# Optimization experiments

Hardware: AMD Instinct MI355X
Metric: run time of the kernel (lower is better)

## Reference

```python
import jax, jax.numpy as jnp
import numpy as np

K = 3          # number of nearest neighbors for interpolation
EPS = 1e-8     # inverse-distance epsilon
BN_EPS = 1e-5  # torch BatchNorm1d default eps

B, NY, NX = 4, 16384, 4096
CY, CX = 128, 256
DIM = CY + CX
SHARED = (512, 256, 128)


def setup_inputs() -> dict:
    key = jax.random.key(0)
    ks = jax.random.split(key, 16)
    inp = {
        'y_points': jax.random.normal(ks[0], (B, NY, 3), jnp.float32),
        'y_feats': jax.random.normal(ks[1], (B, NY, CY), jnp.float32),
        'x_points': jax.random.normal(ks[2], (B, NX, 3), jnp.float32),
        'x_feats': jax.random.normal(ks[3], (B, NX, CX), jnp.float32),
    }
    in_chs = (DIM,) + SHARED[:-1]
    for i, (cin, cout) in enumerate(zip(in_chs, SHARED), start=1):
        scale = 1.0 / np.sqrt(cin)
        inp[f'W{i}'] = jax.random.normal(ks[4 + i], (cout, cin), jnp.float32) * scale
        inp[f'b{i}'] = jnp.zeros((cout,), jnp.float32)
        inp[f'g{i}'] = jnp.ones((cout,), jnp.float32)
        inp[f'be{i}'] = jnp.zeros((cout,), jnp.float32)
    return inp


def _interpolate(y_points, x_points, y_feats, x_feats):
    # squared pairwise distances [B, Ny, Nx]
    d = (jnp.sum(y_points * y_points, -1)[:, :, None]
         + jnp.sum(x_points * x_points, -1)[:, None, :]
         - 2.0 * jnp.einsum('bnd,bmd->bnm', y_points, x_points))
    neg_d, idx = jax.lax.top_k(-d, K)             # K smallest distances
    dists = -neg_d                                 # [B, Ny, K]
    w = 1.0 / (dists + EPS)
    w = w / jnp.sum(w, -1, keepdims=True)
    # gather neighbor features: [B, Ny, K, Cx]
    nb = jnp.take_along_axis(x_feats[:, None, :, :], idx[..., None], axis=2)
    interp = jnp.sum(nb * w[..., None], axis=2)    # [B, Ny, Cx]
    return jnp.concatenate([y_feats, interp], axis=-1)


def _conv_bn_relu(y, W, b, g, beta):
    # 1x1 Conv1d == per-point linear; y: [B, Cin, N]
    y = jnp.einsum('oc,bcn->bon', W, y) + b[None, :, None]
    mu = jnp.mean(y, axis=(0, 2), keepdims=True)
    var = jnp.var(y, axis=(0, 2), keepdims=True)
    y = (y - mu) * jax.lax.rsqrt(var + BN_EPS)
    return jax.nn.relu(y * g[None, :, None] + beta[None, :, None])


def reference(y_points, y_feats, x_points, x_feats,
              W1, b1, g1, be1, W2, b2, g2, be2, W3, b3, g3, be3):
    i_points = _interpolate(y_points, x_points, y_feats, x_feats)  # [B, Ny, DIM]
    y = jnp.transpose(i_points, (0, 2, 1))                          # [B, DIM, Ny]
    y = _conv_bn_relu(y, W1, b1, g1, be1)
    y = _conv_bn_relu(y, W2, b2, g2, be2)
    y = _conv_bn_relu(y, W3, b3, g3, be3)
    return y
```

## Files before the change

kernel.cpp:

```cpp
#include <hip/hip_runtime.h>

#define NYTOT 16384
#define NXP 4096
#define MTOT 65536
#define CYC 128
#define CXC 256
#define DIMC 384

typedef __attribute__((ext_vector_type(8))) _Float16 half8;
typedef __attribute__((ext_vector_type(4))) _Float16 half4;
typedef __attribute__((ext_vector_type(4))) float floatx4;
typedef __attribute__((ext_vector_type(2))) float floatx2;

using half_t = _Float16;

struct alignas(16) HF8 { half_t h[8]; };

__device__ __forceinline__ float fmed3(float a, float b, float c) {
  return __builtin_amdgcn_fmed3f(a, b, c);
}

__global__ __launch_bounds__(1024) void xq_prep(
    const float* __restrict__ x_points, float4* __restrict__ xq) {
#pragma clang fp contract(off)
  int j = blockIdx.x * 1024 + threadIdx.x;
  int b = j >> 12, jj = j & 4095;
  const float* p = x_points + (size_t)b * NXP * 3 + 3 * jj;
  float x0 = p[0], x1 = p[1], x2 = p[2];
  float sx = (x0 * x0 + x1 * x1) + x2 * x2;
  float4 v; v.x = x0; v.y = x1; v.z = x2; v.w = sx;
  xq[j] = v;
}

__global__ __launch_bounds__(1024, 8) void interp_kernel(
    const float* __restrict__ y_points, const float* __restrict__ y_feats,
    const float* __restrict__ x_feats, const float4* __restrict__ xq,
    half_t* __restrict__ A0) {
#pragma clang fp contract(off)
  __shared__ float pd[16][128][3];
  __shared__ int   pi[16][128][3];
  __shared__ float t2s[128];
  __shared__ float sw[3][128];
  __shared__ int   si[3][128];
  const int b = blockIdx.x >> 7;
  const int chunk = blockIdx.x & 127;
  const int t = threadIdx.x;
  const int lane = t & 63;
  const int seg = t >> 6;
  const int yloc = lane << 1;

  const float* yp = y_points + ((size_t)b * NYTOT + chunk * 128 + yloc) * 3;
  floatx2 Y0 = {yp[0], yp[3]};
  floatx2 Y1 = {yp[1], yp[4]};
  floatx2 Y2 = {yp[2], yp[5]};
  floatx2 SY = (Y0 * Y0 + Y1 * Y1) + Y2 * Y2;

  const float4* xqs = xq + (size_t)b * NXP;
  const int jb = __builtin_amdgcn_readfirstlane(seg * 256);

  floatx2 D0 = {1e30f, 1e30f}, D1 = D0, D2 = D0;
#pragma unroll 8
  for (int jj = 0; jj < 256; ++jj) {
    float4 p = xqs[jb + jj];
    floatx2 inner = (Y0 * p.x + Y1 * p.y) + Y2 * p.z;
    floatx2 d = (SY + p.w) - 2.0f * inner;
    D2.x = fmed3(d.x, D1.x, D2.x);  D2.y = fmed3(d.y, D1.y, D2.y);
    D1.x = fmed3(d.x, D0.x, D1.x);  D1.y = fmed3(d.y, D0.y, D1.y);
    D0.x = fminf(d.x, D0.x);        D0.y = fminf(d.y, D0.y);
  }
  pd[seg][yloc][0] = D0.x; pd[seg][yloc][1] = D1.x; pd[seg][yloc][2] = D2.x;
  pd[seg][yloc + 1][0] = D0.y; pd[seg][yloc + 1][1] = D1.y; pd[seg][yloc + 1][2] = D2.y;
  __syncthreads();

  if (t < 128) {
    float m0 = 1e30f, m1 = 1e30f, m2 = 1e30f;
#pragma unroll
    for (int s = 0; s < 16; ++s)
#pragma unroll
      for (int c = 0; c < 3; ++c) {
        float v = pd[s][t][c];
        m2 = fmed3(v, m1, m2);
        m1 = fmed3(v, m0, m1);
        m0 = fminf(v, m0);
      }
    t2s[t] = m2;
  }
  __syncthreads();

  const float t2a = t2s[yloc], t2b = t2s[yloc + 1];
  const float tmax = fmaxf(t2a, t2b);
  float e0a = 1e30f, e1a = 1e30f, e2a = 1e30f; int k0a = 0, k1a = 0, k2a = 0;
  float e0b = 1e30f, e1b = 1e30f, e2b = 1e30f; int k0b = 0, k1b = 0, k2b = 0;
#pragma unroll 4
  for (int jj = 0; jj < 256; ++jj) {
    float4 p = xqs[jb + jj];
    floatx2 inner = (Y0 * p.x + Y1 * p.y) + Y2 * p.z;
    floatx2 d = (SY + p.w) - 2.0f * inner;
    if (fminf(d.x, d.y) <= tmax) {
      int j = jb + jj;
      {
        float dv = d.x;
        bool l0 = dv < e0a, l1 = dv < e1a, l2 = dv < e2a;
        e2a = l1 ? e1a : (l2 ? dv : e2a);  k2a = l1 ? k1a : (l2 ? j : k2a);
        e1a = l0 ? e0a : (l1 ? dv : e1a);  k1a = l0 ? k0a : (l1 ? j : k1a);
        e0a = l0 ? dv : e0a;               k0a = l0 ? j : k0a;
      }
      {
        float dv = d.y;
        bool l0 = dv < e0b, l1 = dv < e1b, l2 = dv < e2b;
        e2b = l1 ? e1b : (l2 ? dv : e2b);  k2b = l1 ? k1b : (l2 ? j : k2b);
        e1b = l0 ? e0b : (l1 ? dv : e1b);  k1b = l0 ? k0b : (l1 ? j : k1b);
        e0b = l0 ? dv : e0b;               k0b = l0 ? j : k0b;
      }
    }
  }
  pd[seg][yloc][0] = e0a; pd[seg][yloc][1] = e1a; pd[seg][yloc][2] = e2a;
  pi[seg][yloc][0] = k0a; pi[seg][yloc][1] = k1a; pi[seg][yloc][2] = k2a;
  pd[seg][yloc + 1][0] = e0b; pd[seg][yloc + 1][1] = e1b; pd[seg][yloc + 1][2] = e2b;
  pi[seg][yloc + 1][0] = k0b; pi[seg][yloc + 1][1] = k1b; pi[seg][yloc + 1][2] = k2b;
  __syncthreads();

  if (t < 128) {
    float f0 = 1e30f, f1 = 1e30f, f2 = 1e30f;
    int m0i = 0, m1i = 0, m2i = 0;
#pragma unroll
    for (int s = 0; s < 16; ++s)
#pragma unroll
      for (int c = 0; c < 3; ++c) {
        float d = pd[s][t][c]; int j = pi[s][t][c];
        bool l0 = d < f0, l1 = d < f1, l2 = d < f2;
        f2 = l1 ? f1 : (l2 ? d : f2);  m2i = l1 ? m1i : (l2 ? j : m2i);
        f1 = l0 ? f0 : (l1 ? d : f1);  m1i = l0 ? m0i : (l1 ? j : m1i);
        f0 = l0 ? d : f0;              m0i = l0 ? j : m0i;
      }
    float w0 = 1.0f / (f0 + 1e-8f), w1 = 1.0f / (f1 + 1e-8f), w2 = 1.0f / (f2 + 1e-8f);
    float ws = (w0 + w1) + w2;
    sw[0][t] = w0 / ws; sw[1][t] = w1 / ws; sw[2][t] = w2 / ws;
    si[0][t] = m0i; si[1][t] = m1i; si[2][t] = m2i;
  }
  __syncthreads();

  const floatx4* xf4 = (const floatx4*)(x_feats + (size_t)b * NXP * CXC);
  const floatx4* yf4 = (const floatx4*)(y_feats + ((size_t)b * NYTOT + chunk * 128) * CYC);
  half_t* fb = A0 + ((size_t)b * NYTOT + chunk * 128) * DIMC;
  {
    const int q = t & 63;
    const int ysub = t >> 6;
    for (int y2 = ysub; y2 < 128; y2 += 16) {
      int j0 = si[0][y2], j1 = si[1][y2], j2 = si[2][y2];
      float a0 = sw[0][y2], a1 = sw[1][y2], a2 = sw[2][y2];
      floatx4 v0 = xf4[(size_t)j0 * 64 + q];
      floatx4 v1 = xf4[(size_t)j1 * 64 + q];
      floatx4 v2 = xf4[(size_t)j2 * 64 + q];
      half4 h;
#pragma unroll
      for (int e = 0; e < 4; ++e)
        h[e] = (half_t)fmaf(v2[e], a2, fmaf(v1[e], a1, v0[e] * a0));
      *(half4*)&fb[(size_t)y2 * DIMC + CYC + q * 4] = h;
    }
  }
  {
    const int q2 = t & 31;
    const int ysub2 = t >> 5;
    for (int y2 = ysub2; y2 < 128; y2 += 32) {
      floatx4 v = yf4[(size_t)y2 * 32 + q2];
      half4 h;
#pragma unroll
      for (int e = 0; e < 4; ++e) h[e] = (half_t)v[e];
      *(half4*)&fb[(size_t)y2 * DIMC + q2 * 4] = h;
    }
  }
}

__global__ __launch_bounds__(256) void wcvt_kernel(
    const float* __restrict__ W1, const float* __restrict__ W2,
    const float* __restrict__ W3, half_t* __restrict__ out) {
  int i = blockIdx.x * 256 + threadIdx.x;
  const float* src; half_t* dst; int j;
  if (i < 49152)      { src = W1; dst = out;          j = i; }
  else if (i < 81920) { src = W2; dst = out + 196608; j = i - 49152; }
  else                { src = W3; dst = out + 327680; j = i - 81920; }
  floatx4 v = ((const floatx4*)src)[j];
  half4 h;
#pragma unroll
  for (int e = 0; e < 4; ++e) h[e] = (half_t)v[e];
  ((half4*)dst)[j] = h;
}

template<int K, int O, int NTN, bool FUSEA>
__global__ __launch_bounds__(512) void gemm256(
    const half_t* __restrict__ A, const half_t* __restrict__ Wh,
    const float* __restrict__ bias, half_t* __restrict__ C,
    float* __restrict__ sums, const float* __restrict__ ssA) {
  __shared__ __align__(16) short As[16][2][512];
  __shared__ __align__(16) short Bs[8][2][512];
  constexpr int NWG = (MTOT / 256) * NTN;
  const int lin = (blockIdx.x & 7) * (NWG >> 3) + (blockIdx.x >> 3);
  const int m0 = (lin / NTN) * 256;
  const int n0 = (lin % NTN) * 128;
  const int tid = threadIdx.x;
  const int lane = tid & 63;
  const int wid = tid >> 6;
  const int wm = wid >> 1, wn = wid & 1;
  const int lm = lane & 15;
  const int lk = (lane >> 4) * 8;
  floatx4 acc[4][4] = {};

  for (int k0 = 0; k0 < K; k0 += 64) {
    __syncthreads();
    if constexpr (FUSEA) {
#pragma unroll
      for (int c = 0; c < 2; ++c) {
        int id = wid * 2 + c;
        int sub = id >> 1, ks = id & 1;
        const half_t* src = Wh + (size_t)(n0 + sub * 16 + lm) * K + (k0 + ks * 32 + lk);
        __builtin_amdgcn_global_load_lds(
            (const __attribute__((address_space(1))) void*)src,
            (__attribute__((address_space(3))) void*)&Bs[sub][ks][0], 16, 0, 0);
      }
      const int r = tid & 255;
      const int hh = tid >> 8;
      const half_t* arow = A + (size_t)(m0 + r) * K + k0 + hh * 32;
      half8 in[4];
#pragma unroll
      for (int g = 0; g < 4; ++g) in[g] = *(const half8*)&arow[g * 8];
#pragma unroll
      for (int g = 0; g < 4; ++g) {
        int kc = k0 + hh * 32 + g * 8;
        half8 h;
#pragma unroll
        for (int e = 0; e < 8; ++e) {
          float f = fmaxf((float)in[g][e] * ssA[kc + e] + ssA[K + kc + e], 0.f);
          h[e] = (half_t)f;
        }
        *(half8*)&As[r >> 4][hh][(g * 16 + (r & 15)) * 8] = h;
      }
    } else {
#pragma unroll
      for (int c = 0; c < 6; ++c) {
        int id = wid * 6 + c;
        if (id < 32) {
          int sub = id >> 1, ks = id & 1;
          const half_t* src = A + (size_t)(m0 + sub * 16 + lm) * K + (k0 + ks * 32 + lk);
          __builtin_amdgcn_global_load_lds(
              (const __attribute__((address_space(1))) void*)src,
              (__attribute__((address_space(3))) void*)&As[sub][ks][0], 16, 0, 0);
        } else {
          int id2 = id - 32;
          int sub = id2 >> 1, ks = id2 & 1;
          const half_t* src = Wh + (size_t)(n0 + sub * 16 + lm) * K + (k0 + ks * 32 + lk);
          __builtin_amdgcn_global_load_lds(
              (const __attribute__((address_space(1))) void*)src,
              (__attribute__((address_space(3))) void*)&Bs[sub][ks][0], 16, 0, 0);
        }
      }
    }
    __syncthreads();
#pragma unroll
    for (int ks = 0; ks < 2; ++ks) {
      half8 af[4], bfm[4];
#pragma unroll
      for (int i = 0; i < 4; ++i) af[i] = *(const half8*)&As[wm * 4 + i][ks][lane * 8];
#pragma unroll
      for (int j = 0; j < 4; ++j) bfm[j] = *(const half8*)&Bs[wn * 4 + j][ks][lane * 8];
#pragma unroll
      for (int i = 0; i < 4; ++i)
#pragma unroll
        for (int j = 0; j < 4; ++j)
          acc[i][j] = __builtin_amdgcn_mfma_f32_16x16x32_f16(af[i], bfm[j], acc[i][j], 0, 0, 0);
    }
  }

#pragma unroll
  for (int j = 0; j < 4; ++j) {
    int nn = n0 + wn * 64 + j * 16 + lm;
    float bv = bias[nn];
    float psum = 0.f, psq = 0.f;
#pragma unroll
    for (int i = 0; i < 4; ++i) {
      int mr = m0 + wm * 64 + i * 16 + (lane >> 4) * 4;
#pragma unroll
      for (int rr = 0; rr < 4; ++rr) {
        float z = acc[i][j][rr] + bv;
        C[(size_t)(mr + rr) * O + nn] = (half_t)z;
        psum += z; psq += z * z;
      }
    }
    psum += __shfl_xor(psum, 16, 64); psq += __shfl_xor(psq, 16, 64);
    psum += __shfl_xor(psum, 32, 64); psq += __shfl_xor(psq, 32, 64);
    if ((lane >> 4) == 0) {
      atomicAdd(&sums[nn], psum);
      atomicAdd(&sums[O + nn], psq);
    }
  }
}

template<int K, int O, bool FUSEA>
__global__ __launch_bounds__(256) void gemm_f16(
    const half_t* __restrict__ A, const half_t* __restrict__ Wh,
    const float* __restrict__ bias, half_t* __restrict__ C,
    float* __restrict__ sums, const float* __restrict__ ssA) {
  __shared__ __align__(16) short As[8][2][512];
  __shared__ __align__(16) short Bs[8][2][512];
  const int m0 = blockIdx.x * 128;
  const int n0 = blockIdx.y * 128;
  const int tid = threadIdx.x;
  const int lane = tid & 63;
  const int wid = tid >> 6;
  const int wm = wid >> 1, wn = wid & 1;
  const int lm = lane & 15;
  const int lk = (lane >> 4) * 8;
  floatx4 acc[4][4] = {};

  for (int k0 = 0; k0 < K; k0 += 64) {
    __syncthreads();
    if constexpr (FUSEA) {
#pragma unroll
      for (int c = 0; c < 4; ++c) {
        int id = wid * 4 + c;
        int sub = id >> 1;
        int ks = id & 1;
        const half_t* src = Wh + (size_t)(n0 + sub * 16 + lm) * K + (k0 + ks * 32 + lk);
        __builtin_amdgcn_global_load_lds(
            (const __attribute__((address_space(1))) void*)src,
            (__attribute__((address_space(3))) void*)&Bs[sub][ks][0], 16, 0, 0);
      }
      const int r = tid & 127;
      const int hh = tid >> 7;
      const half_t* arow = A + (size_t)(m0 + r) * K + k0 + hh * 32;
      half8 in[4];
#pragma unroll
      for (int g = 0; g < 4; ++g) in[g] = *(const half8*)&arow[g * 8];
#pragma unroll
      for (int g = 0; g < 4; ++g) {
        int kc = k0 + hh * 32 + g * 8;
        half8 h;
#pragma unroll
        for (int e = 0; e < 8; ++e) {
          float f = fmaxf((float)in[g][e] * ssA[kc + e] + ssA[K + kc + e], 0.f);
          h[e] = (half_t)f;
        }
        *(half8*)&As[r >> 4][hh][(g * 16 + (r & 15)) * 8] = h;
      }
    } else {
#pragma unroll
      for (int c = 0; c < 8; ++c) {
        int id = wid * 8 + c;
        int sub = (id >> 1) & 7;
        int ks = id & 1;
        const half_t* src = (id < 16)
            ? A  + (size_t)(m0 + sub * 16 + lm) * K + (k0 + ks * 32 + lk)
            : Wh + (size_t)(n0 + sub * 16 + lm) * K + (k0 + ks * 32 + lk);
        __builtin_amdgcn_global_load_lds(
            (const __attribute__((address_space(1))) void*)src,
            (__attribute__((address_space(3))) void*)(id < 16 ? &As[sub][ks][0]
                                                             : &Bs[sub][ks][0]),
            16, 0, 0);
      }
    }
    __syncthreads();
#pragma unroll
    for (int ks = 0; ks < 2; ++ks) {
      half8 af[4], bfm[4];
#pragma unroll
      for (int i = 0; i < 4; ++i) af[i] = *(const half8*)&As[wm * 4 + i][ks][lane * 8];
#pragma unroll
      for (int j = 0; j < 4; ++j) bfm[j] = *(const half8*)&Bs[wn * 4 + j][ks][lane * 8];
#pragma unroll
      for (int i = 0; i < 4; ++i)
#pragma unroll
        for (int j = 0; j < 4; ++j)
          acc[i][j] = __builtin_amdgcn_mfma_f32_16x16x32_f16(af[i], bfm[j], acc[i][j], 0, 0, 0);
    }
  }

#pragma unroll
  for (int j = 0; j < 4; ++j) {
    int nn = n0 + wn * 64 + j * 16 + lm;
    float bv = bias[nn];
    float psum = 0.f, psq = 0.f;
#pragma unroll
    for (int i = 0; i < 4; ++i) {
      int mr = m0 + wm * 64 + i * 16 + (lane >> 4) * 4;
#pragma unroll
      for (int rr = 0; rr < 4; ++rr) {
        float z = acc[i][j][rr] + bv;
        C[(size_t)(mr + rr) * O + nn] = (half_t)z;
        psum += z; psq += z * z;
      }
    }
    psum += __shfl_xor(psum, 16, 64); psq += __shfl_xor(psq, 16, 64);
    psum += __shfl_xor(psum, 32, 64); psq += __shfl_xor(psq, 32, 64);
    if ((lane >> 4) == 0) {
      atomicAdd(&sums[nn], psum);
      atomicAdd(&sums[O + nn], psq);
    }
  }
}

__global__ void finalize_kernel(const float* __restrict__ sums, const float* __restrict__ g,
                                const float* __restrict__ be, float* __restrict__ ss, int O) {
  int c = threadIdx.x;
  if (c < O) {
    const float invN = 1.0f / 65536.0f;
    float mean = sums[c] * invN;
    float var = sums[O + c] * invN - mean * mean;
    float sc = g[c] / sqrtf(var + 1e-5f);
    float sh = be[c] - mean * sc;
    if (!isfinite(sc) || !isfinite(sh)) { sc = 1.0f; sh = 0.0f; }
    ss[c] = sc;
    ss[O + c] = sh;
  }
}

__global__ __launch_bounds__(256) void bn_transpose_kernel(
    const half_t* __restrict__ Z3, const float* __restrict__ ss, float* __restrict__ out) {
  __shared__ float tile[64][129];
  const int r0 = blockIdx.x * 64;
  const int b = r0 >> 14;
  const int n0 = r0 & (NYTOT - 1);
  const int t = threadIdx.x;
  const int cl = t & 127, rl = t >> 7;
  for (int p = 0; p < 32; ++p) {
    int rr = p * 2 + rl;
    float v = (float)Z3[(size_t)(r0 + rr) * 128 + cl];
    tile[rr][cl] = fmaxf(v * ss[cl] + ss[128 + cl], 0.f);
  }
  __syncthreads();
  const int nl = t & 63, cj = t >> 6;
  for (int p = 0; p < 32; ++p) {
    int c = p * 4 + cj;
    out[(size_t)b * 128 * NYTOT + (size_t)c * NYTOT + n0 + nl] = tile[nl][c];
  }
}

extern "C" void kernel_launch(void* const* d_in, const int* in_sizes, int n_in,
                              void* d_out, int out_size, void* d_ws, size_t ws_size,
                              hipStream_t stream) {
  const float* y_points = (const float*)d_in[0];
  const float* y_feats  = (const float*)d_in[1];
  const float* x_points = (const float*)d_in[2];
  const float* x_feats  = (const float*)d_in[3];
  const float* W1 = (const float*)d_in[4];  const float* b1 = (const float*)d_in[5];
  const float* g1 = (const float*)d_in[6];  const float* be1 = (const float*)d_in[7];
  const float* W2 = (const float*)d_in[8];  const float* b2 = (const float*)d_in[9];
  const float* g2 = (const float*)d_in[10]; const float* be2 = (const float*)d_in[11];
  const float* W3 = (const float*)d_in[12]; const float* b3 = (const float*)d_in[13];
  const float* g3 = (const float*)d_in[14]; const float* be3 = (const float*)d_in[15];

  char* ws = (char*)d_ws;
  half_t* A0 = (half_t*)ws;
  half_t* z1 = (half_t*)(ws + 50331648);
  half_t* z2 = (half_t*)ws;
  half_t* z3 = (half_t*)(ws + 50331648);
  float4* xq = (float4*)(ws + 50331648);
  float* st = (float*)(ws + 117440512);
  half_t* W1h = (half_t*)d_out;
  half_t* W2h = W1h + 196608;
  half_t* W3h = W1h + 327680;
  hipMemsetAsync(st, 0, 1792 * sizeof(float), stream);

  xq_prep<<<16, 1024, 0, stream>>>(x_points, xq);
  wcvt_kernel<<<352, 256, 0, stream>>>(W1, W2, W3, W1h);
  interp_kernel<<<512, 1024, 0, stream>>>(y_points, y_feats, x_feats, xq, A0);

  gemm256<384, 512, 4, false><<<1024, 512, 0, stream>>>(A0, W1h, b1, z1, st + 0, nullptr);
  finalize_kernel<<<1, 512, 0, stream>>>(st + 0, g1, be1, st + 1792, 512);

  gemm256<512, 256, 2, true><<<512, 512, 0, stream>>>(z1, W2h, b2, z2, st + 1024, st + 1792);
  finalize_kernel<<<1, 256, 0, stream>>>(st + 1024, g2, be2, st + 2816, 256);

  gemm_f16<256, 128, true><<<dim3(512, 1), 256, 0, stream>>>(z2, W3h, b3, z3, st + 1536, st + 2816);
  finalize_kernel<<<1, 128, 0, stream>>>(st + 1536, g3, be3, st + 3328, 128);

  bn_transpose_kernel<<<1024, 256, 0, stream>>>(z3, st + 3328, (float*)d_out);
}
```

Baseline: 461.6 us.

## Use packed-f32 SoA distance math and replace BN stat atomics with partial buffers

The x-point table moves from an AoS float4 layout to SoA planes, so each loop iteration loads pairs of candidate points as 64-bit scalar-broadcast operands. Distances are computed with inline-asm v_pk_mul/v_pk_add f32, handling two candidates per instruction in both the threshold and selection passes. The GEMM epilogues now write per-wave partial sums and sums of squares into scratch buffers held inside the output tensor, instead of issuing global float atomics. A parallel finalize kernel reduces those partials, which also removes the memset. The trade-off is extra partial-buffer traffic and a 1024-row reduction per channel in finalize, plus inline asm that constrains compiler scheduling.

```diff
diff --git a/kernel.cpp b/kernel.cpp
--- a/kernel.cpp
+++ b/kernel.cpp
@@ -11,6 +11,8 @@
 typedef __attribute__((ext_vector_type(4))) _Float16 half4;
 typedef __attribute__((ext_vector_type(4))) float floatx4;
 typedef __attribute__((ext_vector_type(2))) float floatx2;
+typedef __attribute__((ext_vector_type(2))) float f2;
+typedef unsigned long long u64c;
 
 using half_t = _Float16;
 
@@ -20,21 +22,44 @@
   return __builtin_amdgcn_fmed3f(a, b, c);
 }
 
+__device__ __forceinline__ f2 pkmul_sv(u64c s, f2 v) {
+  f2 r; asm("v_pk_mul_f32 %0, %1, %2" : "=v"(r) : "s"(s), "v"(v)); return r;
+}
+__device__ __forceinline__ f2 pkadd_sv(u64c s, f2 v) {
+  f2 r; asm("v_pk_add_f32 %0, %1, %2" : "=v"(r) : "s"(s), "v"(v)); return r;
+}
+__device__ __forceinline__ f2 pkmul_vv(f2 a, f2 b) {
+  f2 r; asm("v_pk_mul_f32 %0, %1, %2" : "=v"(r) : "v"(a), "v"(b)); return r;
+}
+__device__ __forceinline__ f2 pkadd_vv(f2 a, f2 b) {
+  f2 r; asm("v_pk_add_f32 %0, %1, %2" : "=v"(r) : "v"(a), "v"(b)); return r;
+}
+__device__ __forceinline__ f2 pkdist(u64c px, u64c py, u64c pz, u64c pw,
+                                     f2 y0, f2 y1, f2 y2, f2 sy, f2 m2) {
+  f2 t0 = pkmul_sv(px, y0);
+  f2 t1 = pkmul_sv(py, y1);
+  f2 s01 = pkadd_vv(t0, t1);
+  f2 t2 = pkmul_sv(pz, y2);
+  f2 inner = pkadd_vv(s01, t2);
+  f2 u = pkadd_sv(pw, sy);
+  f2 w = pkmul_vv(inner, m2);
+  return pkadd_vv(u, w);
+}
+
 __global__ __launch_bounds__(1024) void xq_prep(
-    const float* __restrict__ x_points, float4* __restrict__ xq) {
+    const float* __restrict__ x_points, float* __restrict__ XS) {
 #pragma clang fp contract(off)
   int j = blockIdx.x * 1024 + threadIdx.x;
   int b = j >> 12, jj = j & 4095;
   const float* p = x_points + (size_t)b * NXP * 3 + 3 * jj;
   float x0 = p[0], x1 = p[1], x2 = p[2];
   float sx = (x0 * x0 + x1 * x1) + x2 * x2;
-  float4 v; v.x = x0; v.y = x1; v.z = x2; v.w = sx;
-  xq[j] = v;
+  XS[j] = x0; XS[16384 + j] = x1; XS[32768 + j] = x2; XS[49152 + j] = sx;
 }
 
 __global__ __launch_bounds__(1024, 8) void interp_kernel(
     const float* __restrict__ y_points, const float* __restrict__ y_feats,
-    const float* __restrict__ x_feats, const float4* __restrict__ xq,
+    const float* __restrict__ x_feats, const float* __restrict__ XS,
     half_t* __restrict__ A0) {
 #pragma clang fp contract(off)
   __shared__ float pd[16][128][3];
@@ -55,35 +80,45 @@
   floatx2 Y2 = {yp[2], yp[5]};
   floatx2 SY = (Y0 * Y0 + Y1 * Y1) + Y2 * Y2;
 
-  const float4* xqs = xq + (size_t)b * NXP;
+  f2 y0a = {Y0.x, Y0.x}, y1a = {Y1.x, Y1.x}, y2a = {Y2.x, Y2.x}, sya = {SY.x, SY.x};
+  f2 y0b = {Y0.y, Y0.y}, y1b = {Y1.y, Y1.y}, y2b = {Y2.y, Y2.y}, syb = {SY.y, SY.y};
+  f2 m2 = {-2.0f, -2.0f};
+
+  const int boff = b * 4096;
   const int jb = __builtin_amdgcn_readfirstlane(seg * 256);
-
-  floatx2 D0 = {1e30f, 1e30f}, D1 = D0, D2 = D0;
-#pragma unroll 8
-  for (int jj = 0; jj < 256; ++jj) {
-    float4 p = xqs[jb + jj];
-    floatx2 inner = (Y0 * p.x + Y1 * p.y) + Y2 * p.z;
-    floatx2 d = (SY + p.w) - 2.0f * inner;
-    D2.x = fmed3(d.x, D1.x, D2.x);  D2.y = fmed3(d.y, D1.y, D2.y);
-    D1.x = fmed3(d.x, D0.x, D1.x);  D1.y = fmed3(d.y, D0.y, D1.y);
-    D0.x = fminf(d.x, D0.x);        D0.y = fminf(d.y, D0.y);
-  }
-  pd[seg][yloc][0] = D0.x; pd[seg][yloc][1] = D1.x; pd[seg][yloc][2] = D2.x;
-  pd[seg][yloc + 1][0] = D0.y; pd[seg][yloc + 1][1] = D1.y; pd[seg][yloc + 1][2] = D2.y;
+  const u64c* PX = (const u64c*)(XS + boff + jb);
+  const u64c* PY = (const u64c*)(XS + 16384 + boff + jb);
+  const u64c* PZ = (const u64c*)(XS + 32768 + boff + jb);
+  const u64c* PW = (const u64c*)(XS + 49152 + boff + jb);
+
+  float D0a = 1e30f, D1a = 1e30f, D2a = 1e30f;
+  float D0b = 1e30f, D1b = 1e30f, D2b = 1e30f;
+#pragma unroll 4
+  for (int i2 = 0; i2 < 128; ++i2) {
+    u64c px = PX[i2], py = PY[i2], pz = PZ[i2], pw = PW[i2];
+    f2 dA = pkdist(px, py, pz, pw, y0a, y1a, y2a, sya, m2);
+    f2 dB = pkdist(px, py, pz, pw, y0b, y1b, y2b, syb, m2);
+    D2a = fmed3(dA[0], D1a, D2a); D1a = fmed3(dA[0], D0a, D1a); D0a = fminf(dA[0], D0a);
+    D2b = fmed3(dB[0], D1b, D2b); D1b = fmed3(dB[0], D0b, D1b); D0b = fminf(dB[0], D0b);
+    D2a = fmed3(dA[1], D1a, D2a); D1a = fmed3(dA[1], D0a, D1a); D0a = fminf(dA[1], D0a);
+    D2b = fmed3(dB[1], D1b, D2b); D1b = fmed3(dB[1], D0b, D1b); D0b = fminf(dB[1], D0b);
+  }
+  pd[seg][yloc][0] = D0a; pd[seg][yloc][1] = D1a; pd[seg][yloc][2] = D2a;
+  pd[seg][yloc + 1][0] = D0b; pd[seg][yloc + 1][1] = D1b; pd[seg][yloc + 1][2] = D2b;
   __syncthreads();
 
   if (t < 128) {
-    float m0 = 1e30f, m1 = 1e30f, m2 = 1e30f;
+    float m0 = 1e30f, m1 = 1e30f, m2v = 1e30f;
 #pragma unroll
     for (int s = 0; s < 16; ++s)
 #pragma unroll
       for (int c = 0; c < 3; ++c) {
         float v = pd[s][t][c];
-        m2 = fmed3(v, m1, m2);
+        m2v = fmed3(v, m1, m2v);
         m1 = fmed3(v, m0, m1);
         m0 = fminf(v, m0);
       }
-    t2s[t] = m2;
+    t2s[t] = m2v;
   }
   __syncthreads();
 
@@ -91,29 +126,32 @@
   const float tmax = fmaxf(t2a, t2b);
   float e0a = 1e30f, e1a = 1e30f, e2a = 1e30f; int k0a = 0, k1a = 0, k2a = 0;
   float e0b = 1e30f, e1b = 1e30f, e2b = 1e30f; int k0b = 0, k1b = 0, k2b = 0;
-#pragma unroll 4
-  for (int jj = 0; jj < 256; ++jj) {
-    float4 p = xqs[jb + jj];
-    floatx2 inner = (Y0 * p.x + Y1 * p.y) + Y2 * p.z;
-    floatx2 d = (SY + p.w) - 2.0f * inner;
-    if (fminf(d.x, d.y) <= tmax) {
-      int j = jb + jj;
-      {
-        float dv = d.x;
-        bool l0 = dv < e0a, l1 = dv < e1a, l2 = dv < e2a;
-        e2a = l1 ? e1a : (l2 ? dv : e2a);  k2a = l1 ? k1a : (l2 ? j : k2a);
-        e1a = l0 ? e0a : (l1 ? dv : e1a);  k1a = l0 ? k0a : (l1 ? j : k1a);
-        e0a = l0 ? dv : e0a;               k0a = l0 ? j : k0a;
-      }
-      {
-        float dv = d.y;
-        bool l0 = dv < e0b, l1 = dv < e1b, l2 = dv < e2b;
-        e2b = l1 ? e1b : (l2 ? dv : e2b);  k2b = l1 ? k1b : (l2 ? j : k2b);
-        e1b = l0 ? e0b : (l1 ? dv : e1b);  k1b = l0 ? k0b : (l1 ? j : k1b);
-        e0b = l0 ? dv : e0b;               k0b = l0 ? j : k0b;
-      }
-    }
-  }
+#define UPD3(dv, e0, e1, e2, k0, k1, k2, jv)                                 \
+  { bool l0 = dv < e0, l1 = dv < e1, l2 = dv < e2;                           \
+    e2 = l1 ? e1 : (l2 ? dv : e2);  k2 = l1 ? k1 : (l2 ? jv : k2);           \
+    e1 = l0 ? e0 : (l1 ? dv : e1);  k1 = l0 ? k0 : (l1 ? jv : k1);           \
+    e0 = l0 ? dv : e0;              k0 = l0 ? jv : k0; }
+#pragma unroll 2
+  for (int i2 = 0; i2 < 128; ++i2) {
+    u64c px = PX[i2], py = PY[i2], pz = PZ[i2], pw = PW[i2];
+    f2 dA = pkdist(px, py, pz, pw, y0a, y1a, y2a, sya, m2);
+    f2 dB = pkdist(px, py, pz, pw, y0b, y1b, y2b, syb, m2);
+    float g0 = fminf(dA[0], dB[0]);
+    float g1 = fminf(dA[1], dB[1]);
+    if (fminf(g0, g1) <= tmax) {
+      int j = jb + 2 * i2;
+      if (g0 <= tmax) {
+        UPD3(dA[0], e0a, e1a, e2a, k0a, k1a, k2a, j);
+        UPD3(dB[0], e0b, e1b, e2b, k0b, k1b, k2b, j);
+      }
+      if (g1 <= tmax) {
+        int j1 = j + 1;
+        UPD3(dA[1], e0a, e1a, e2a, k0a, k1a, k2a, j1);
+        UPD3(dB[1], e0b, e1b, e2b, k0b, k1b, k2b, j1);
+      }
+    }
+  }
+#undef UPD3
   pd[seg][yloc][0] = e0a; pd[seg][yloc][1] = e1a; pd[seg][yloc][2] = e2a;
   pi[seg][yloc][0] = k0a; pi[seg][yloc][1] = k1a; pi[seg][yloc][2] = k2a;
   pd[seg][yloc + 1][0] = e0b; pd[seg][yloc + 1][1] = e1b; pd[seg][yloc + 1][2] = e2b;
@@ -121,19 +159,19 @@
   __syncthreads();
 
   if (t < 128) {
-    float f0 = 1e30f, f1 = 1e30f, f2 = 1e30f;
+    float f0 = 1e30f, f1 = 1e30f, f2v = 1e30f;
     int m0i = 0, m1i = 0, m2i = 0;
 #pragma unroll
     for (int s = 0; s < 16; ++s)
 #pragma unroll
       for (int c = 0; c < 3; ++c) {
         float d = pd[s][t][c]; int j = pi[s][t][c];
-        bool l0 = d < f0, l1 = d < f1, l2 = d < f2;
-        f2 = l1 ? f1 : (l2 ? d : f2);  m2i = l1 ? m1i : (l2 ? j : m2i);
-        f1 = l0 ? f0 : (l1 ? d : f1);  m1i = l0 ? m0i : (l1 ? j : m1i);
-        f0 = l0 ? d : f0;              m0i = l0 ? j : m0i;
-      }
-    float w0 = 1.0f / (f0 + 1e-8f), w1 = 1.0f / (f1 + 1e-8f), w2 = 1.0f / (f2 + 1e-8f);
+        bool l0 = d < f0, l1 = d < f1, l2 = d < f2v;
+        f2v = l1 ? f1 : (l2 ? d : f2v);  m2i = l1 ? m1i : (l2 ? j : m2i);
+        f1 = l0 ? f0 : (l1 ? d : f1);    m1i = l0 ? m0i : (l1 ? j : m1i);
+        f0 = l0 ? d : f0;                m0i = l0 ? j : m0i;
+      }
+    float w0 = 1.0f / (f0 + 1e-8f), w1 = 1.0f / (f1 + 1e-8f), w2 = 1.0f / (f2v + 1e-8f);
     float ws = (w0 + w1) + w2;
     sw[0][t] = w0 / ws; sw[1][t] = w1 / ws; sw[2][t] = w2 / ws;
     si[0][t] = m0i; si[1][t] = m1i; si[2][t] = m2i;
@@ -191,7 +229,7 @@
 __global__ __launch_bounds__(512) void gemm256(
     const half_t* __restrict__ A, const half_t* __restrict__ Wh,
     const float* __restrict__ bias, half_t* __restrict__ C,
-    float* __restrict__ sums, const float* __restrict__ ssA) {
+    float* __restrict__ P, const float* __restrict__ ssA) {
   __shared__ __align__(16) short As[16][2][512];
   __shared__ __align__(16) short Bs[8][2][512];
   constexpr int NWG = (MTOT / 256) * NTN;
@@ -271,6 +309,7 @@
     }
   }
 
+  float* Pr = P + (size_t)((m0 >> 8) * 4 + wm) * (2 * O);
 #pragma unroll
   for (int j = 0; j < 4; ++j) {
     int nn = n0 + wn * 64 + j * 16 + lm;
@@ -289,8 +328,8 @@
     psum += __shfl_xor(psum, 16, 64); psq += __shfl_xor(psq, 16, 64);
     psum += __shfl_xor(psum, 32, 64); psq += __shfl_xor(psq, 32, 64);
     if ((lane >> 4) == 0) {
-      atomicAdd(&sums[nn], psum);
-      atomicAdd(&sums[O + nn], psq);
+      Pr[nn] = psum;
+      Pr[O + nn] = psq;
     }
   }
 }
@@ -299,7 +338,7 @@
 __global__ __launch_bounds__(256) void gemm_f16(
     const half_t* __restrict__ A, const half_t* __restrict__ Wh,
     const float* __restrict__ bias, half_t* __restrict__ C,
-    float* __restrict__ sums, const float* __restrict__ ssA) {
+    float* __restrict__ P, const float* __restrict__ ssA) {
   __shared__ __align__(16) short As[8][2][512];
   __shared__ __align__(16) short Bs[8][2][512];
   const int m0 = blockIdx.x * 128;
@@ -374,6 +413,7 @@
     }
   }
 
+  float* Pr = P + (size_t)((m0 >> 7) * 2 + wm) * (2 * O);
 #pragma unroll
   for (int j = 0; j < 4; ++j) {
     int nn = n0 + wn * 64 + j * 16 + lm;
@@ -392,25 +432,31 @@
     psum += __shfl_xor(psum, 16, 64); psq += __shfl_xor(psq, 16, 64);
     psum += __shfl_xor(psum, 32, 64); psq += __shfl_xor(psq, 32, 64);
     if ((lane >> 4) == 0) {
-      atomicAdd(&sums[nn], psum);
-      atomicAdd(&sums[O + nn], psq);
-    }
-  }
-}
-
-__global__ void finalize_kernel(const float* __restrict__ sums, const float* __restrict__ g,
-                                const float* __restrict__ be, float* __restrict__ ss, int O) {
-  int c = threadIdx.x;
-  if (c < O) {
-    const float invN = 1.0f / 65536.0f;
-    float mean = sums[c] * invN;
-    float var = sums[O + c] * invN - mean * mean;
-    float sc = g[c] / sqrtf(var + 1e-5f);
-    float sh = be[c] - mean * sc;
-    if (!isfinite(sc) || !isfinite(sh)) { sc = 1.0f; sh = 0.0f; }
-    ss[c] = sc;
-    ss[O + c] = sh;
-  }
+      Pr[nn] = psum;
+      Pr[O + nn] = psq;
+    }
+  }
+}
+
+__global__ __launch_bounds__(64) void finalize_kernel(
+    const float* __restrict__ P, const float* __restrict__ g,
+    const float* __restrict__ be, float* __restrict__ ss, int O, int R) {
+  int c = blockIdx.x * 64 + threadIdx.x;
+  if (c >= O) return;
+  float sum = 0.f, sq = 0.f;
+#pragma unroll 4
+  for (int r = 0; r < R; ++r) {
+    sum += P[(size_t)r * 2 * O + c];
+    sq  += P[(size_t)r * 2 * O + O + c];
+  }
+  const float invN = 1.0f / 65536.0f;
+  float mean = sum * invN;
+  float var = sq * invN - mean * mean;
+  float sc = g[c] / sqrtf(var + 1e-5f);
+  float sh = be[c] - mean * sc;
+  if (!isfinite(sc) || !isfinite(sh)) { sc = 1.0f; sh = 0.0f; }
+  ss[c] = sc;
+  ss[O + c] = sh;
 }
 
 __global__ __launch_bounds__(256) void bn_transpose_kernel(
@@ -453,25 +499,27 @@
   half_t* z1 = (half_t*)(ws + 50331648);
   half_t* z2 = (half_t*)ws;
   half_t* z3 = (half_t*)(ws + 50331648);
-  float4* xq = (float4*)(ws + 50331648);
+  float*  XS = (float*)(ws + 50331648);
   float* st = (float*)(ws + 117440512);
   half_t* W1h = (half_t*)d_out;
   half_t* W2h = W1h + 196608;
   half_t* W3h = W1h + 327680;
-  hipMemsetAsync(st, 0, 1792 * sizeof(float), stream);
-
-  xq_prep<<<16, 1024, 0, stream>>>(x_points, xq);
+  float* P1 = (float*)((char*)d_out + 8388608);
+  float* P2 = (float*)((char*)d_out + 12582912);
+  float* P3 = (float*)((char*)d_out + 14680064);
+
+  xq_prep<<<16, 1024, 0, stream>>>(x_points, XS);
   wcvt_kernel<<<352, 256, 0, stream>>>(W1, W2, W3, W1h);
-  interp_kernel<<<512, 1024, 0, stream>>>(y_points, y_feats, x_feats, xq, A0);
-
-  gemm256<384, 512, 4, false><<<1024, 512, 0, stream>>>(A0, W1h, b1, z1, st + 0, nullptr);
-  finalize_kernel<<<1, 512, 0, stream>>>(st + 0, g1, be1, st + 1792, 512);
-
-  gemm256<512, 256, 2, true><<<512, 512, 0, stream>>>(z1, W2h, b2, z2, st + 1024, st + 1792);
-  finalize_kernel<<<1, 256, 0, stream>>>(st + 1024, g2, be2, st + 2816, 256);
-
-  gemm_f16<256, 128, true><<<dim3(512, 1), 256, 0, stream>>>(z2, W3h, b3, z3, st + 1536, st + 2816);
-  finalize_kernel<<<1, 128, 0, stream>>>(st + 1536, g3, be3, st + 3328, 128);
-
-  bn_transpose_kernel<<<1024, 256, 0, stream>>>(z3, st + 3328, (float*)d_out);
-}
+  interp_kernel<<<512, 1024, 0, stream>>>(y_points, y_feats, x_feats, XS, A0);
+
+  gemm256<384, 512, 4, false><<<1024, 512, 0, stream>>>(A0, W1h, b1, z1, P1, nullptr);
+  finalize_kernel<<<8, 64, 0, stream>>>(P1, g1, be1, st + 0, 512, 1024);
+
+  gemm256<512, 256, 2, true><<<512, 512, 0, stream>>>(z1, W2h, b2, z2, P2, st + 0);
+  finalize_kernel<<<4, 64, 0, stream>>>(P2, g2, be2, st + 1024, 256, 1024);
+
+  gemm_f16<256, 128, true><<<dim3(512, 1), 256, 0, stream>>>(z2, W3h, b3, z3, P3, st + 1024);
+  finalize_kernel<<<2, 64, 0, stream>>>(P3, g3, be3, st + 1536, 128, 1024);
+
+  bn_transpose_kernel<<<1024, 256, 0, stream>>>(z3, st + 1536, (float*)d_out);
+}
```

Measured after the change: 646.7 us. +40.1%, slower.

## Write transposed layer-3 output from GEMM epilogue and merge prep kernels

Applied to the files above, without the earlier changes.

The last GEMM now writes its pre-BN output directly in channel-major [B, C, N] layout using half4 stores. This lets the final BN+ReLU pass become a simple vectorized elementwise kernel instead of a shared-memory transpose. Separately, the x-point prep and weight conversion kernels are merged into one launch to cut launch overhead. The transposed epilogue stores are strided by NYTOT per channel, which may coalesce less well than the previous row-major writes.

```diff
diff --git a/kernel.cpp b/kernel.cpp
--- a/kernel.cpp
+++ b/kernel.cpp
@@ -20,16 +20,32 @@
   return __builtin_amdgcn_fmed3f(a, b, c);
 }
 
-__global__ __launch_bounds__(1024) void xq_prep(
-    const float* __restrict__ x_points, float4* __restrict__ xq) {
+__global__ __launch_bounds__(256) void prep_kernel(
+    const float* __restrict__ x_points, float4* __restrict__ xq,
+    const float* __restrict__ W1, const float* __restrict__ W2,
+    const float* __restrict__ W3, half_t* __restrict__ wout) {
 #pragma clang fp contract(off)
-  int j = blockIdx.x * 1024 + threadIdx.x;
-  int b = j >> 12, jj = j & 4095;
-  const float* p = x_points + (size_t)b * NXP * 3 + 3 * jj;
-  float x0 = p[0], x1 = p[1], x2 = p[2];
-  float sx = (x0 * x0 + x1 * x1) + x2 * x2;
-  float4 v; v.x = x0; v.y = x1; v.z = x2; v.w = sx;
-  xq[j] = v;
+  const int bid = blockIdx.x;
+  if (bid < 64) {
+    int j = bid * 256 + threadIdx.x;
+    int b = j >> 12, jj = j & 4095;
+    const float* p = x_points + (size_t)b * NXP * 3 + 3 * jj;
+    float x0 = p[0], x1 = p[1], x2 = p[2];
+    float sx = (x0 * x0 + x1 * x1) + x2 * x2;
+    float4 v; v.x = x0; v.y = x1; v.z = x2; v.w = sx;
+    xq[j] = v;
+  } else {
+    int i = (bid - 64) * 256 + threadIdx.x;
+    const float* src; half_t* dst; int j;
+    if (i < 49152)      { src = W1; dst = wout;          j = i; }
+    else if (i < 81920) { src = W2; dst = wout + 196608; j = i - 49152; }
+    else                { src = W3; dst = wout + 327680; j = i - 81920; }
+    floatx4 v = ((const floatx4*)src)[j];
+    half4 h;
+#pragma unroll
+    for (int e = 0; e < 4; ++e) h[e] = (half_t)v[e];
+    ((half4*)dst)[j] = h;
+  }
 }
 
 __global__ __launch_bounds__(1024, 8) void interp_kernel(
@@ -170,21 +186,6 @@
       *(half4*)&fb[(size_t)y2 * DIMC + q2 * 4] = h;
     }
   }
-}
-
-__global__ __launch_bounds__(256) void wcvt_kernel(
-    const float* __restrict__ W1, const float* __restrict__ W2,
-    const float* __restrict__ W3, half_t* __restrict__ out) {
-  int i = blockIdx.x * 256 + threadIdx.x;
-  const float* src; half_t* dst; int j;
-  if (i < 49152)      { src = W1; dst = out;          j = i; }
-  else if (i < 81920) { src = W2; dst = out + 196608; j = i - 49152; }
-  else                { src = W3; dst = out + 327680; j = i - 81920; }
-  floatx4 v = ((const floatx4*)src)[j];
-  half4 h;
-#pragma unroll
-  for (int e = 0; e < 4; ++e) h[e] = (half_t)v[e];
-  ((half4*)dst)[j] = h;
 }
 
 template<int K, int O, int NTN, bool FUSEA>
@@ -295,7 +296,7 @@
   }
 }
 
-template<int K, int O, bool FUSEA>
+template<int K, int O, bool FUSEA, bool TOUT>
 __global__ __launch_bounds__(256) void gemm_f16(
     const half_t* __restrict__ A, const half_t* __restrict__ Wh,
     const float* __restrict__ bias, half_t* __restrict__ C,
@@ -374,6 +375,8 @@
     }
   }
 
+  const int bb = m0 >> 14;
+  const int nbase = (m0 & (NYTOT - 1)) + wm * 64 + (lane >> 4) * 4;
 #pragma unroll
   for (int j = 0; j < 4; ++j) {
     int nn = n0 + wn * 64 + j * 16 + lm;
@@ -381,12 +384,20 @@
     float psum = 0.f, psq = 0.f;
 #pragma unroll
     for (int i = 0; i < 4; ++i) {
-      int mr = m0 + wm * 64 + i * 16 + (lane >> 4) * 4;
+      half4 hv;
 #pragma unroll
       for (int rr = 0; rr < 4; ++rr) {
         float z = acc[i][j][rr] + bv;
-        C[(size_t)(mr + rr) * O + nn] = (half_t)z;
+        hv[rr] = (half_t)z;
         psum += z; psq += z * z;
+      }
+      if constexpr (TOUT) {
+        *(half4*)&C[((size_t)(bb * O + nn)) * NYTOT + nbase + i * 16] = hv;
+      } else {
+        int mr = m0 + wm * 64 + i * 16 + (lane >> 4) * 4;
+#pragma unroll
+        for (int rr = 0; rr < 4; ++rr)
+          C[(size_t)(mr + rr) * O + nn] = hv[rr];
       }
     }
     psum += __shfl_xor(psum, 16, 64); psq += __shfl_xor(psq, 16, 64);
@@ -413,25 +424,21 @@
   }
 }
 
-__global__ __launch_bounds__(256) void bn_transpose_kernel(
-    const half_t* __restrict__ Z3, const float* __restrict__ ss, float* __restrict__ out) {
-  __shared__ float tile[64][129];
-  const int r0 = blockIdx.x * 64;
-  const int b = r0 >> 14;
-  const int n0 = r0 & (NYTOT - 1);
-  const int t = threadIdx.x;
-  const int cl = t & 127, rl = t >> 7;
-  for (int p = 0; p < 32; ++p) {
-    int rr = p * 2 + rl;
-    float v = (float)Z3[(size_t)(r0 + rr) * 128 + cl];
-    tile[rr][cl] = fmaxf(v * ss[cl] + ss[128 + cl], 0.f);
-  }
-  __syncthreads();
-  const int nl = t & 63, cj = t >> 6;
-  for (int p = 0; p < 32; ++p) {
-    int c = p * 4 + cj;
-    out[(size_t)b * 128 * NYTOT + (size_t)c * NYTOT + n0 + nl] = tile[nl][c];
-  }
+__global__ __launch_bounds__(256) void bnfin_kernel(
+    const half_t* __restrict__ Z, const float* __restrict__ ss,
+    float* __restrict__ out) {
+  size_t i = (size_t)blockIdx.x * 256 + threadIdx.x;
+  int c = (int)((i * 8) >> 14) & 127;
+  float sc = ss[c], sh = ss[128 + c];
+  HF8 v = ((const HF8*)Z)[i];
+  floatx4 o0, o1;
+#pragma unroll
+  for (int e = 0; e < 4; ++e) {
+    o0[e] = fmaxf((float)v.h[e] * sc + sh, 0.f);
+    o1[e] = fmaxf((float)v.h[4 + e] * sc + sh, 0.f);
+  }
+  ((floatx4*)out)[i * 2] = o0;
+  ((floatx4*)out)[i * 2 + 1] = o1;
 }
 
 extern "C" void kernel_launch(void* const* d_in, const int* in_sizes, int n_in,
@@ -452,7 +459,7 @@
   half_t* A0 = (half_t*)ws;
   half_t* z1 = (half_t*)(ws + 50331648);
   half_t* z2 = (half_t*)ws;
-  half_t* z3 = (half_t*)(ws + 50331648);
+  half_t* z3T = (half_t*)(ws + 50331648);
   float4* xq = (float4*)(ws + 50331648);
   float* st = (float*)(ws + 117440512);
   half_t* W1h = (half_t*)d_out;
@@ -460,8 +467,7 @@
   half_t* W3h = W1h + 327680;
   hipMemsetAsync(st, 0, 1792 * sizeof(float), stream);
 
-  xq_prep<<<16, 1024, 0, stream>>>(x_points, xq);
-  wcvt_kernel<<<352, 256, 0, stream>>>(W1, W2, W3, W1h);
+  prep_kernel<<<416, 256, 0, stream>>>(x_points, xq, W1, W2, W3, W1h);
   interp_kernel<<<512, 1024, 0, stream>>>(y_points, y_feats, x_feats, xq, A0);
 
   gemm256<384, 512, 4, false><<<1024, 512, 0, stream>>>(A0, W1h, b1, z1, st + 0, nullptr);
@@ -470,8 +476,8 @@
   gemm256<512, 256, 2, true><<<512, 512, 0, stream>>>(z1, W2h, b2, z2, st + 1024, st + 1792);
   finalize_kernel<<<1, 256, 0, stream>>>(st + 1024, g2, be2, st + 2816, 256);
 
-  gemm_f16<256, 128, true><<<dim3(512, 1), 256, 0, stream>>>(z2, W3h, b3, z3, st + 1536, st + 2816);
+  gemm_f16<256, 128, true, true><<<dim3(512, 1), 256, 0, stream>>>(z2, W3h, b3, z3T, st + 1536, st + 2816);
   finalize_kernel<<<1, 128, 0, stream>>>(st + 1536, g3, be3, st + 3328, 128);
 
-  bn_transpose_kernel<<<1024, 256, 0, stream>>>(z3, st + 3328, (float*)d_out);
-}
+  bnfin_kernel<<<4096, 256, 0, stream>>>(z3T, st + 3328, (float*)d_out);
+}
```

New measurement: 460.9 us. No clear change (-0.2%).
